# Kernel optimization log

Hardware: AMD Instinct MI355X
Metric: run time of the kernel (lower is better)

The kernel has to match this reference:

```python
import jax, jax.numpy as jnp
import numpy as np

DIM = 768
NUM_EXPERTS = 8


def setup_inputs() -> dict:
    key = jax.random.key(0)
    k_x, k_w, k_b = jax.random.split(key, 3)
    x = jax.random.normal(k_x, (128, 197, DIM), dtype=jnp.float32)
    # nn.Linear(dim, num_experts): weight [num_experts, dim], bias [num_experts]
    bound = 1.0 / np.sqrt(DIM)
    W = jax.random.uniform(k_w, (NUM_EXPERTS, DIM), minval=-bound, maxval=bound, dtype=jnp.float32)
    b = jax.random.uniform(k_b, (NUM_EXPERTS,), minval=-bound, maxval=bound, dtype=jnp.float32)
    return {"x": x, "W": W, "b": b}


def reference(x, W, b):
    # gate projection: [B, S, E]
    logits = jnp.einsum("bsd,ed->bse", x, W) + b
    gates = jax.nn.softmax(logits, axis=-1)
    topk_gates, topk_idx = jax.lax.top_k(gates, 2)  # [B, S, 2] each
    return (topk_gates, topk_idx)
```

## Files before the change

### kernel.cpp

```cpp
#include <hip/hip_runtime.h>

#define DIM 768
#define NE 8
#define NTOK (128 * 197)
#define TPW 8
#define NWAVES (NTOK / TPW)

__global__ __launch_bounds__(64) void router_kernel(
    const float* __restrict__ x,
    const float* __restrict__ W,
    const float* __restrict__ b,
    float* __restrict__ out)
{
    const int lane = threadIdx.x;
    const int wave = blockIdx.x;

    const int l3 = lane & 7;
    const int e_lane = ((l3 & 1) << 2) | (l3 & 2) | ((l3 >> 2) & 1);

    float4 wreg[NE][3];
#pragma unroll
    for (int e = 0; e < NE; ++e) {
#pragma unroll
        for (int c = 0; c < 3; ++c) {
            wreg[e][c] = *reinterpret_cast<const float4*>(W + e * DIM + c * 256 + lane * 4);
        }
    }
    const float bias = b[e_lane];

    int tok = wave * TPW;
    const float* xp = x + (size_t)tok * DIM + lane * 4;

    float4 cx0 = *reinterpret_cast<const float4*>(xp);
    float4 cx1 = *reinterpret_cast<const float4*>(xp + 256);
    float4 cx2 = *reinterpret_cast<const float4*>(xp + 512);

    for (int t = 0; t < TPW; ++t, ++tok) {
        const float* xn = xp + DIM;
        float4 nx0, nx1, nx2;
        if (t + 1 < TPW) {
            nx0 = *reinterpret_cast<const float4*>(xn);
            nx1 = *reinterpret_cast<const float4*>(xn + 256);
            nx2 = *reinterpret_cast<const float4*>(xn + 512);
        } else {
            nx0 = nx1 = nx2 = make_float4(0.f, 0.f, 0.f, 0.f);
        }

        float acc[NE];
#pragma unroll
        for (int e = 0; e < NE; ++e) {
            float a;
            a = cx0.x * wreg[e][0].x;
            a = fmaf(cx0.y, wreg[e][0].y, a);
            a = fmaf(cx0.z, wreg[e][0].z, a);
            a = fmaf(cx0.w, wreg[e][0].w, a);
            a = fmaf(cx1.x, wreg[e][1].x, a);
            a = fmaf(cx1.y, wreg[e][1].y, a);
            a = fmaf(cx1.z, wreg[e][1].z, a);
            a = fmaf(cx1.w, wreg[e][1].w, a);
            a = fmaf(cx2.x, wreg[e][2].x, a);
            a = fmaf(cx2.y, wreg[e][2].y, a);
            a = fmaf(cx2.z, wreg[e][2].z, a);
            a = fmaf(cx2.w, wreg[e][2].w, a);
            acc[e] = a;
        }

        float r4[4];
        {
            const bool hi = (lane & 1) != 0;
#pragma unroll
            for (int k = 0; k < 4; ++k) {
                float send = hi ? acc[k] : acc[k + 4];
                float recv = __shfl_xor(send, 1, 64);
                r4[k] = (hi ? acc[k + 4] : acc[k]) + recv;
            }
        }
        float r2[2];
        {
            const bool hi = (lane & 2) != 0;
#pragma unroll
            for (int k = 0; k < 2; ++k) {
                float send = hi ? r2[0] * 0.f + r4[k] : r4[k + 2];
                send = hi ? r4[k] : r4[k + 2];
                float recv = __shfl_xor(send, 2, 64);
                r2[k] = (hi ? r4[k + 2] : r4[k]) + recv;
            }
        }
        float lg;
        {
            const bool hi = (lane & 4) != 0;
            float send = hi ? r2[0] : r2[1];
            float recv = __shfl_xor(send, 4, 64);
            lg = (hi ? r2[1] : r2[0]) + recv;
        }
        lg += __shfl_xor(lg, 8, 64);
        lg += __shfl_xor(lg, 16, 64);
        lg += __shfl_xor(lg, 32, 64);
        lg += bias;

        float logit[NE];
#pragma unroll
        for (int e = 0; e < NE; ++e) {
            const int src = ((e & 1) << 2) | (e & 2) | ((e >> 2) & 1);
            logit[e] = __shfl(lg, src, 64);
        }

        float v1 = logit[0]; int i1 = 0;
        float v2 = -1e30f;   int i2 = 0;
#pragma unroll
        for (int e = 1; e < NE; ++e) {
            const float v = logit[e];
            const bool gt1 = v > v1;
            const bool gt2 = v > v2;
            v2 = gt1 ? v1 : (gt2 ? v : v2);
            i2 = gt1 ? i1 : (gt2 ? e : i2);
            v1 = gt1 ? v : v1;
            i1 = gt1 ? e : i1;
        }

        float Z = 0.f;
#pragma unroll
        for (int e = 0; e < NE; ++e) Z += __expf(logit[e] - v1);
        const float g1 = 1.0f / Z;
        const float g2 = __expf(v2 - v1) / Z;

        if (lane == 0) {
            reinterpret_cast<float2*>(out)[tok] = make_float2(g1, g2);
        } else if (lane == 1) {
            reinterpret_cast<float2*>(out + 2 * (size_t)NTOK)[tok] =
                make_float2((float)i1, (float)i2);
        }

        cx0 = nx0; cx1 = nx1; cx2 = nx2;
        xp = xn;
    }
}

extern "C" void kernel_launch(void* const* d_in, const int* in_sizes, int n_in,
                              void* d_out, int out_size, void* d_ws, size_t ws_size,
                              hipStream_t stream) {
    const float* x = (const float*)d_in[0];
    const float* W = (const float*)d_in[1];
    const float* b = (const float*)d_in[2];
    float* out = (float*)d_out;
    (void)in_sizes; (void)n_in; (void)out_size; (void)d_ws; (void)ws_size;

    router_kernel<<<NWAVES, 64, 0, stream>>>(x, W, b, out);
}
```

Measured before the change: 113.8 us.

## Pack four waves per block and batch per-token output stores

Launches 256-thread blocks holding four independent waves instead of one-wave blocks, with launch bounds targeting three blocks per CU. Each lane now keeps the result for one token in registers and all eight tokens' outputs are written together at the end, replacing per-iteration scattered stores. The next-token prefetch is made unconditional by reloading the current row on the last iteration, which removes a branch but adds redundant loads. The launch-bounds hint may constrain registers and cause spilling of the 96-register weight cache.

```diff
diff --git a/kernel.cpp b/kernel.cpp
--- a/kernel.cpp
+++ b/kernel.cpp
@@ -5,15 +5,17 @@
 #define NTOK (128 * 197)
 #define TPW 8
 #define NWAVES (NTOK / TPW)
+#define WPB 4
+#define NBLK (NWAVES / WPB)
 
-__global__ __launch_bounds__(64) void router_kernel(
+__global__ __launch_bounds__(256, 3) void router_kernel(
     const float* __restrict__ x,
     const float* __restrict__ W,
     const float* __restrict__ b,
     float* __restrict__ out)
 {
-    const int lane = threadIdx.x;
-    const int wave = blockIdx.x;
+    const int lane = threadIdx.x & 63;
+    const int wave = blockIdx.x * WPB + (threadIdx.x >> 6);
 
     const int l3 = lane & 7;
     const int e_lane = ((l3 & 1) << 2) | (l3 & 2) | ((l3 >> 2) & 1);
@@ -28,23 +30,21 @@
     }
     const float bias = b[e_lane];
 
-    int tok = wave * TPW;
-    const float* xp = x + (size_t)tok * DIM + lane * 4;
+    const int tok0 = wave * TPW;
+    const float* xp = x + (size_t)tok0 * DIM + lane * 4;
 
     float4 cx0 = *reinterpret_cast<const float4*>(xp);
     float4 cx1 = *reinterpret_cast<const float4*>(xp + 256);
     float4 cx2 = *reinterpret_cast<const float4*>(xp + 512);
 
-    for (int t = 0; t < TPW; ++t, ++tok) {
-        const float* xn = xp + DIM;
-        float4 nx0, nx1, nx2;
-        if (t + 1 < TPW) {
-            nx0 = *reinterpret_cast<const float4*>(xn);
-            nx1 = *reinterpret_cast<const float4*>(xn + 256);
-            nx2 = *reinterpret_cast<const float4*>(xn + 512);
-        } else {
-            nx0 = nx1 = nx2 = make_float4(0.f, 0.f, 0.f, 0.f);
-        }
+    float2 rg = make_float2(0.f, 0.f);
+    float2 ri = make_float2(0.f, 0.f);
+
+    for (int t = 0; t < TPW; ++t) {
+        const float* xn = (t + 1 < TPW) ? xp + DIM : xp;
+        float4 nx0 = *reinterpret_cast<const float4*>(xn);
+        float4 nx1 = *reinterpret_cast<const float4*>(xn + 256);
+        float4 nx2 = *reinterpret_cast<const float4*>(xn + 512);
 
         float acc[NE];
 #pragma unroll
@@ -80,8 +80,7 @@
             const bool hi = (lane & 2) != 0;
 #pragma unroll
             for (int k = 0; k < 2; ++k) {
-                float send = hi ? r2[0] * 0.f + r4[k] : r4[k + 2];
-                send = hi ? r4[k] : r4[k + 2];
+                float send = hi ? r4[k] : r4[k + 2];
                 float recv = __shfl_xor(send, 2, 64);
                 r2[k] = (hi ? r4[k + 2] : r4[k]) + recv;
             }
@@ -124,15 +123,18 @@
         const float g1 = 1.0f / Z;
         const float g2 = __expf(v2 - v1) / Z;
 
-        if (lane == 0) {
-            reinterpret_cast<float2*>(out)[tok] = make_float2(g1, g2);
-        } else if (lane == 1) {
-            reinterpret_cast<float2*>(out + 2 * (size_t)NTOK)[tok] =
-                make_float2((float)i1, (float)i2);
+        if (lane == t) {
+            rg = make_float2(g1, g2);
+            ri = make_float2((float)i1, (float)i2);
         }
 
         cx0 = nx0; cx1 = nx1; cx2 = nx2;
         xp = xn;
+    }
+
+    if (lane < TPW) {
+        reinterpret_cast<float2*>(out)[tok0 + lane] = rg;
+        reinterpret_cast<float2*>(out + 2 * (size_t)NTOK)[tok0 + lane] = ri;
     }
 }
 
@@ -145,5 +147,5 @@
     float* out = (float*)d_out;
     (void)in_sizes; (void)n_in; (void)out_size; (void)d_ws; (void)ws_size;
 
-    router_kernel<<<NWAVES, 64, 0, stream>>>(x, W, b, out);
+    router_kernel<<<NBLK, WPB * 64, 0, stream>>>(x, W, b, out);
 }
```

New measurement: 110.8 us (median of 2 runs). 2.7% less time.
